# Kernel tuning notes

Hardware: AMD Instinct MI355X
Metric: run time of the kernel (lower is better)

The kernel has to match this reference:

```python
import jax, jax.numpy as jnp
import numpy as np

NEG_SLOPE = 0.01  # torch leaky_relu default

def _leaky_relu(x):
    return jnp.where(x >= 0, x, NEG_SLOPE * x)

def setup_inputs() -> dict:
    key = jax.random.key(0)
    ks = jax.random.split(key, 12)
    n_drug, n_disease, n_edges, d = 10000, 10000, 1000000, 100
    inp = {
        "x_drug": jax.random.normal(ks[0], (n_drug, d), dtype=jnp.float32),
        "x_disease": jax.random.normal(ks[1], (n_disease, d), dtype=jnp.float32),
        "edge_label_index": jax.random.randint(ks[2], (2, n_edges), 0, n_drug, dtype=jnp.int64),
        "W1": jax.random.normal(ks[3], (200, 128), dtype=jnp.float32) * 0.07,
        "b1": jax.random.normal(ks[4], (128,), dtype=jnp.float32) * 0.01,
        "W2": jax.random.normal(ks[5], (128, 32), dtype=jnp.float32) * 0.09,
        "b2": jax.random.normal(ks[6], (32,), dtype=jnp.float32) * 0.01,
        "W3": jax.random.normal(ks[7], (32, 16), dtype=jnp.float32) * 0.18,
        "b3": jax.random.normal(ks[8], (16,), dtype=jnp.float32) * 0.01,
        "W4": jax.random.normal(ks[9], (16, 1), dtype=jnp.float32) * 0.25,
        "b4": jax.random.normal(ks[10], (1,), dtype=jnp.float32) * 0.01,
    }
    return inp

def reference(x_drug, x_disease, edge_label_index, W1, b1, W2, b2, W3, b3, W4, b4):
    # gather per-edge node embeddings and concat -> [E, 200]
    ef = jnp.concatenate([x_drug[edge_label_index[0]],
                          x_disease[edge_label_index[1]]], axis=-1)
    ef = _leaky_relu(ef @ W1 + b1)
    ef = _leaky_relu(ef @ W2 + b2)
    ef = _leaky_relu(ef @ W3 + b3)
    ef = ef @ W4 + b4
    return jnp.squeeze(ef, axis=-1)
```

## Files before the change

### kernel.cpp

```cpp
#include <hip/hip_runtime.h>
#include <cstdint>
#include <cstddef>

typedef _Float16 hf2   __attribute__((ext_vector_type(2)));
typedef _Float16 f16x8 __attribute__((ext_vector_type(8)));
typedef float    f32x4 __attribute__((ext_vector_type(4)));

__device__ __forceinline__ f16x8 q2h8(uint4 q) { union { uint4 q; f16x8 h; } c; c.q = q; return c.h; }
__device__ __forceinline__ hf2 pkrtz(float lo, float hi) {
    auto v = __builtin_amdgcn_cvt_pkrtz(lo, hi);
    union { decltype(v) a; hf2 b; } c; c.a = v; return c.b;
}
__device__ __forceinline__ float lreluf(float x) { return fmaxf(x, 0.01f * x); }
__device__ __forceinline__ f16x8 lrelu8(uint4 a, uint4 b) {
    f16x8 s = q2h8(a) + q2h8(b);
    f16x8 m = s * (_Float16)0.01f;
    return __builtin_elementwise_max(s, m);
}

__global__ __launch_bounds__(256) void node_proj2(
    const float* __restrict__ xd, const float* __restrict__ xi,
    const float* __restrict__ W1, const float* __restrict__ b1,
    _Float16* __restrict__ Pd, _Float16* __restrict__ Pi,
    int nd, int ni, int nblk_d, int nblk_i,
    const float* __restrict__ W2, const float* __restrict__ W3,
    _Float16* __restrict__ W2f, _Float16* __restrict__ W3f,
    const unsigned* __restrict__ ew, long long nwords, int* __restrict__ flag)
{
    const int t = threadIdx.x;
    const int nproj = nblk_d + nblk_i;

    if ((int)blockIdx.x >= nproj) {
        if ((int)blockIdx.x == nproj) {
            for (int idx = t; idx < 4096; idx += 256) {
                int i  = idx & 7;
                int l  = (idx >> 3) & 63;
                int kt = (idx >> 9) & 3;
                int nt = (idx >> 11) & 1;
                int k = kt * 32 + 8 * (l >> 4) + i;
                int j = nt * 16 + (l & 15);
                W2f[idx] = (_Float16)W2[k * 32 + j];
            }
            for (int idx = t; idx < 512; idx += 256) {
                int i = idx & 7, l = idx >> 3;
                W3f[idx] = (_Float16)W3[(8 * (l >> 4) + i) * 16 + (l & 15)];
            }
        } else if (t < 64) {
            const long long pairs = nwords / 2;
            const long long step  = pairs / 64;
            unsigned v = 0;
            for (int s = 0; s < 4; ++s) {
                long long p = (long long)t * step + (long long)s * (step / 4 + 1);
                if (p < pairs) v |= ew[2 * p + 1];
            }
            unsigned long long ball = __ballot(v != 0);
            if (t == 0) *flag = (ball == 0ULL) ? 1 : 0;
        }
        return;
    }

    __shared__ float xs[1600];
    const int c  = t & 127;
    const int ty = t >> 7;
    const bool dis = (int)blockIdx.x >= nblk_d;
    const int b = dis ? (blockIdx.x - nblk_d) : blockIdx.x;
    const int n = dis ? ni : nd;
    const float* x = dis ? xi : xd;
    const float* W = dis ? (W1 + 100 * 128) : W1;
    _Float16* P = dis ? Pi : Pd;
    const float bv = dis ? b1[c] : 0.f;
    const int r0 = b * 16;

    const long long gbase = (long long)r0 * 100;
    const long long lim   = (long long)n * 100;
    for (int idx = t; idx < 1600; idx += 256) {
        long long g = gbase + idx;
        xs[idx] = (g < lim) ? x[g] : 0.f;
    }
    __syncthreads();

    float acc[8];
#pragma unroll
    for (int i = 0; i < 8; ++i) acc[i] = bv;

    const float4* xs4 = (const float4*)xs;
#pragma unroll 5
    for (int kk = 0; kk < 25; ++kk) {
        float w0 = W[(4 * kk + 0) * 128 + c];
        float w1 = W[(4 * kk + 1) * 128 + c];
        float w2 = W[(4 * kk + 2) * 128 + c];
        float w3 = W[(4 * kk + 3) * 128 + c];
#pragma unroll
        for (int i = 0; i < 8; ++i) {
            float4 xv = xs4[(ty * 8 + i) * 25 + kk];
            acc[i] = fmaf(xv.x, w0, acc[i]);
            acc[i] = fmaf(xv.y, w1, acc[i]);
            acc[i] = fmaf(xv.z, w2, acc[i]);
            acc[i] = fmaf(xv.w, w3, acc[i]);
        }
    }
#pragma unroll
    for (int i = 0; i < 8; ++i) {
        int r = r0 + ty * 8 + i;
        if (r < n) P[(size_t)r * 128 + c] = (_Float16)acc[i];
    }
}

__global__ __launch_bounds__(256) void edge_mlp(
    const void* __restrict__ eidx_raw,
    const _Float16* __restrict__ Pd, const _Float16* __restrict__ Pi,
    const _Float16* __restrict__ W2f, const float* __restrict__ b2,
    const _Float16* __restrict__ W3f, const float* __restrict__ b3,
    const float* __restrict__ W4, const float* __restrict__ b4,
    const int* __restrict__ flag64,
    float* __restrict__ out, int E)
{
    __shared__ __align__(16) float H2[4][64 * 36];

    const int t  = threadIdx.x;
    const int l  = t & 63;
    const int w  = t >> 6;
    const int er = l & 15;
    const int cg = l >> 4;
    const int base = blockIdx.x * 256 + w * 64;
    const int e_c = min(base + l, E - 1);
    float* Hw = H2[w];

    int i0, i1;
    if (*flag64) {
        const long long* p = (const long long*)eidx_raw;
        i0 = (int)p[e_c];
        i1 = (int)p[(size_t)E + e_c];
    } else {
        const int* p = (const int*)eidx_raw;
        i0 = p[e_c];
        i1 = p[(size_t)E + e_c];
    }

    f16x8 bf0[4], bf1[4];
    {
        const uint4* W2q = (const uint4*)W2f;
#pragma unroll
        for (int kt = 0; kt < 4; ++kt) {
            bf0[kt] = q2h8(W2q[kt * 64 + l]);
            bf1[kt] = q2h8(W2q[256 + kt * 64 + l]);
        }
    }
    const f16x8 w3f = q2h8(((const uint4*)W3f)[l]);
    const float  b2v0 = b2[er], b2v1 = b2[16 + er];
    const float4 b3q  = ((const float4*)b3)[cg];
    const float4 w4q  = ((const float4*)W4)[cg];
    const float  b4v  = b4[0];

    f32x4 c0[4], c1[4];
#pragma unroll
    for (int q = 0; q < 4; ++q) {
        const int src = q * 16 + er;
        const int j0 = __shfl(i0, src, 64);
        const int j1 = __shfl(i1, src, 64);
        const uint4* rowD = (const uint4*)(Pd + (size_t)j0 * 128);
        const uint4* rowI = (const uint4*)(Pi + (size_t)j1 * 128);
        c0[q] = (f32x4){0.f, 0.f, 0.f, 0.f};
        c1[q] = (f32x4){0.f, 0.f, 0.f, 0.f};
#pragma unroll
        for (int kt = 0; kt < 4; ++kt) {
            f16x8 af = lrelu8(rowD[kt * 4 + cg], rowI[kt * 4 + cg]);
            c0[q] = __builtin_amdgcn_mfma_f32_16x16x32_f16(af, bf0[kt], c0[q], 0, 0, 0);
            c1[q] = __builtin_amdgcn_mfma_f32_16x16x32_f16(af, bf1[kt], c1[q], 0, 0, 0);
        }
    }

#pragma unroll
    for (int q = 0; q < 4; ++q)
#pragma unroll
        for (int r = 0; r < 4; ++r) {
            const int e = q * 16 + 4 * cg + r;
            Hw[e * 36 + er]      = lreluf(c0[q][r] + b2v0);
            Hw[e * 36 + 16 + er] = lreluf(c1[q][r] + b2v1);
        }

#pragma unroll
    for (int q = 0; q < 4; ++q) {
        const int e2 = q * 16 + er;
        const float4* hr = (const float4*)&Hw[e2 * 36 + 8 * cg];
        float4 h0 = hr[0], h1 = hr[1];
        union { hf2 h[4]; f16x8 v; } u;
        u.h[0] = pkrtz(h0.x, h0.y);
        u.h[1] = pkrtz(h0.z, h0.w);
        u.h[2] = pkrtz(h1.x, h1.y);
        u.h[3] = pkrtz(h1.z, h1.w);

        f32x4 d3 = __builtin_amdgcn_mfma_f32_16x16x32_f16(
            w3f, u.v, (f32x4){0.f, 0.f, 0.f, 0.f}, 0, 0, 0);

        float v = lreluf(d3[0] + b3q.x) * w4q.x;
        v      += lreluf(d3[1] + b3q.y) * w4q.y;
        v      += lreluf(d3[2] + b3q.z) * w4q.z;
        v      += lreluf(d3[3] + b3q.w) * w4q.w;
        v += __shfl_xor(v, 16, 64);
        v += __shfl_xor(v, 32, 64);

        if (cg == 0) {
            const int eo = base + q * 16 + er;
            if (eo < E) out[eo] = v + b4v;
        }
    }
}

extern "C" void kernel_launch(void* const* d_in, const int* in_sizes, int n_in,
                              void* d_out, int out_size, void* d_ws, size_t ws_size,
                              hipStream_t stream)
{
    const float* x_drug = (const float*)d_in[0];
    const float* x_dis  = (const float*)d_in[1];
    const void*  eidx   = d_in[2];
    const float* W1 = (const float*)d_in[3];
    const float* b1 = (const float*)d_in[4];
    const float* W2 = (const float*)d_in[5];
    const float* b2 = (const float*)d_in[6];
    const float* W3 = (const float*)d_in[7];
    const float* b3 = (const float*)d_in[8];
    const float* W4 = (const float*)d_in[9];
    const float* b4 = (const float*)d_in[10];

    const int nd = in_sizes[0] / 100;
    const int ni = in_sizes[1] / 100;
    const int E  = in_sizes[2] / 2;

    char* ws = (char*)d_ws;
    _Float16* Pd  = (_Float16*)ws;                   size_t off = (size_t)nd * 128 * 2;
    _Float16* Pi  = (_Float16*)(ws + off);           off += (size_t)ni * 128 * 2;
    _Float16* W2f = (_Float16*)(ws + off);           off += 4096 * 2;
    _Float16* W3f = (_Float16*)(ws + off);           off += 512 * 2;
    int* flag = (int*)(ws + off);

    const int nblk_d = (nd + 15) / 16;
    const int nblk_i = (ni + 15) / 16;

    node_proj2<<<nblk_d + nblk_i + 2, 256, 0, stream>>>(
        x_drug, x_dis, W1, b1, Pd, Pi, nd, ni, nblk_d, nblk_i,
        W2, W3, W2f, W3f,
        (const unsigned*)eidx, 2LL * E, flag);

    edge_mlp<<<(E + 255) / 256, 256, 0, stream>>>(eidx, Pd, Pi,
                                                  W2f, b2, W3f, b3, W4, b4,
                                                  flag, (float*)d_out, E);
}
```

Baseline: 162.9 us.

## Double-buffer edge row gathers, store H2 in fp16 LDS, raise occupancy hint

```diff
diff --git a/kernel.cpp b/kernel.cpp
--- a/kernel.cpp
+++ b/kernel.cpp
@@ -106,7 +106,7 @@
     }
 }
 
-__global__ __launch_bounds__(256) void edge_mlp(
+__global__ __launch_bounds__(256, 4) void edge_mlp(
     const void* __restrict__ eidx_raw,
     const _Float16* __restrict__ Pd, const _Float16* __restrict__ Pi,
     const _Float16* __restrict__ W2f, const float* __restrict__ b2,
@@ -115,7 +115,7 @@
     const int* __restrict__ flag64,
     float* __restrict__ out, int E)
 {
-    __shared__ __align__(16) float H2[4][64 * 36];
+    __shared__ __align__(16) _Float16 H2[4][64 * 40];
 
     const int t  = threadIdx.x;
     const int l  = t & 63;
@@ -124,7 +124,7 @@
     const int cg = l >> 4;
     const int base = blockIdx.x * 256 + w * 64;
     const int e_c = min(base + l, E - 1);
-    float* Hw = H2[w];
+    _Float16* Hw = H2[w];
 
     int i0, i1;
     if (*flag64) {
@@ -137,6 +137,13 @@
         i1 = p[(size_t)E + e_c];
     }
 
+    int j0[4], j1[4];
+#pragma unroll
+    for (int q = 0; q < 4; ++q) {
+        j0[q] = __shfl(i0, q * 16 + er, 64);
+        j1[q] = __shfl(i1, q * 16 + er, 64);
+    }
+
     f16x8 bf0[4], bf1[4];
     {
         const uint4* W2q = (const uint4*)W2f;
@@ -146,52 +153,59 @@
             bf1[kt] = q2h8(W2q[256 + kt * 64 + l]);
         }
     }
-    const f16x8 w3f = q2h8(((const uint4*)W3f)[l]);
-    const float  b2v0 = b2[er], b2v1 = b2[16 + er];
-    const float4 b3q  = ((const float4*)b3)[cg];
-    const float4 w4q  = ((const float4*)W4)[cg];
-    const float  b4v  = b4[0];
-
-    f32x4 c0[4], c1[4];
+    const float b2v0 = b2[er], b2v1 = b2[16 + er];
+
+    uint4 dA[2][4], dB[2][4];
+    {
+        const uint4* rD = (const uint4*)(Pd + (size_t)j0[0] * 128);
+        const uint4* rI = (const uint4*)(Pi + (size_t)j1[0] * 128);
+#pragma unroll
+        for (int kt = 0; kt < 4; ++kt) {
+            dA[0][kt] = rD[kt * 4 + cg];
+            dB[0][kt] = rI[kt * 4 + cg];
+        }
+    }
+
 #pragma unroll
     for (int q = 0; q < 4; ++q) {
-        const int src = q * 16 + er;
-        const int j0 = __shfl(i0, src, 64);
-        const int j1 = __shfl(i1, src, 64);
-        const uint4* rowD = (const uint4*)(Pd + (size_t)j0 * 128);
-        const uint4* rowI = (const uint4*)(Pi + (size_t)j1 * 128);
-        c0[q] = (f32x4){0.f, 0.f, 0.f, 0.f};
-        c1[q] = (f32x4){0.f, 0.f, 0.f, 0.f};
+        if (q < 3) {
+            const uint4* rD = (const uint4*)(Pd + (size_t)j0[q + 1] * 128);
+            const uint4* rI = (const uint4*)(Pi + (size_t)j1[q + 1] * 128);
+#pragma unroll
+            for (int kt = 0; kt < 4; ++kt) {
+                dA[(q + 1) & 1][kt] = rD[kt * 4 + cg];
+                dB[(q + 1) & 1][kt] = rI[kt * 4 + cg];
+            }
+        }
+
+        f32x4 c0 = {0.f, 0.f, 0.f, 0.f}, c1 = {0.f, 0.f, 0.f, 0.f};
 #pragma unroll
         for (int kt = 0; kt < 4; ++kt) {
-            f16x8 af = lrelu8(rowD[kt * 4 + cg], rowI[kt * 4 + cg]);
-            c0[q] = __builtin_amdgcn_mfma_f32_16x16x32_f16(af, bf0[kt], c0[q], 0, 0, 0);
-            c1[q] = __builtin_amdgcn_mfma_f32_16x16x32_f16(af, bf1[kt], c1[q], 0, 0, 0);
-        }
-    }
-
-#pragma unroll
-    for (int q = 0; q < 4; ++q)
+            f16x8 af = lrelu8(dA[q & 1][kt], dB[q & 1][kt]);
+            c0 = __builtin_amdgcn_mfma_f32_16x16x32_f16(af, bf0[kt], c0, 0, 0, 0);
+            c1 = __builtin_amdgcn_mfma_f32_16x16x32_f16(af, bf1[kt], c1, 0, 0, 0);
+        }
+
 #pragma unroll
         for (int r = 0; r < 4; ++r) {
             const int e = q * 16 + 4 * cg + r;
-            Hw[e * 36 + er]      = lreluf(c0[q][r] + b2v0);
-            Hw[e * 36 + 16 + er] = lreluf(c1[q][r] + b2v1);
-        }
+            Hw[e * 40 + er]      = (_Float16)lreluf(c0[r] + b2v0);
+            Hw[e * 40 + 16 + er] = (_Float16)lreluf(c1[r] + b2v1);
+        }
+    }
+
+    const f16x8 w3f = q2h8(((const uint4*)W3f)[l]);
+    const float4 b3q = ((const float4*)b3)[cg];
+    const float4 w4q = ((const float4*)W4)[cg];
+    const float  b4v = b4[0];
 
 #pragma unroll
     for (int q = 0; q < 4; ++q) {
         const int e2 = q * 16 + er;
-        const float4* hr = (const float4*)&Hw[e2 * 36 + 8 * cg];
-        float4 h0 = hr[0], h1 = hr[1];
-        union { hf2 h[4]; f16x8 v; } u;
-        u.h[0] = pkrtz(h0.x, h0.y);
-        u.h[1] = pkrtz(h0.z, h0.w);
-        u.h[2] = pkrtz(h1.x, h1.y);
-        u.h[3] = pkrtz(h1.z, h1.w);
+        f16x8 hv = *(const f16x8*)&Hw[e2 * 40 + 8 * cg];
 
         f32x4 d3 = __builtin_amdgcn_mfma_f32_16x16x32_f16(
-            w3f, u.v, (f32x4){0.f, 0.f, 0.f, 0.f}, 0, 0, 0);
+            w3f, hv, (f32x4){0.f, 0.f, 0.f, 0.f}, 0, 0, 0);
 
         float v = lreluf(d3[0] + b3q.x) * w4q.x;
         v      += lreluf(d3[1] + b3q.y) * w4q.y;
```

New measurement: 161.2 us. Within noise of the previous version (-1.1%).
